# Kernel optimization log

Hardware: AMD Instinct MI355X
Metric: run time of the kernel (lower is better)

## Reference

```python
import jax, jax.numpy as jnp
import numpy as np

N_ENTITIES = 80000
N_EDGES = 1280000
N_RELATIONS = 50
EMB = 64


def setup_inputs() -> dict:
    key = jax.random.key(0)
    k1, k2, k3, k4 = jax.random.split(key, 4)
    entity_emb = jax.random.normal(k1, (N_ENTITIES, EMB), dtype=jnp.float32)
    edge_index = jax.random.randint(k2, (2, N_EDGES), 0, N_ENTITIES, dtype=jnp.int64)
    edge_type = jax.random.randint(k3, (N_EDGES,), 0, N_RELATIONS, dtype=jnp.int64)
    relation_emb = jax.random.normal(k4, (N_RELATIONS, EMB), dtype=jnp.float32)
    return {
        "entity_emb": entity_emb,
        "edge_index": edge_index,
        "edge_type": edge_type,
        "relation_emb": relation_emb,
        "n_entities": N_ENTITIES,
    }


def reference(entity_emb, edge_index, edge_type, relation_emb, n_entities):
    head, tail = edge_index[0], edge_index[1]          # [E], [E]
    rel = relation_emb[edge_type]                      # [E, D] gather
    head_emb = entity_emb[head]                        # [E, D] gather
    tail_emb = entity_emb[tail]                        # [E, D] gather
    # per-edge dot-product score over head * relation * tail
    scores = jnp.sum(head_emb * rel * tail_emb, axis=-1)  # [E]
    # segment softmax over edges grouped by head (numerically stable)
    seg_max = jax.ops.segment_max(scores, head, num_segments=n_entities)  # [N]
    ex = jnp.exp(scores - seg_max[head])                                  # [E]
    seg_sum = jax.ops.segment_sum(ex, head, num_segments=n_entities)     # [N]
    attn = ex / seg_sum[head]                                             # [E]
    # weighted scatter-sum of tail embeddings into head slots
    entity_agg = jax.ops.segment_sum(tail_emb * attn[:, None], head,
                                     num_segments=n_entities)             # [N, D]
    return entity_agg
```

## Files before the change

### kernel.cpp

```cpp
#include <hip/hip_runtime.h>
#include <hip/hip_fp16.h>


#define NBK        1250
#define BCAP       1280
#define EDGE_TILE4 4096

__device__ __forceinline__ int f2i(float x) { return __builtin_bit_cast(int, x); }
__device__ __forceinline__ float i2f(int x) { return __builtin_bit_cast(float, x); }

template <int N>
__device__ __forceinline__ float dpp_ror_add(float x) {
    int y = __builtin_amdgcn_update_dpp(0, f2i(x), 0x120 + N, 0xF, 0xF, true);
    return x + i2f(y);
}
__device__ __forceinline__ float swz16(float x) {
    return i2f(__builtin_amdgcn_ds_swizzle(f2i(x), 0x401F));
}
__device__ __forceinline__ float bperm(int ba, float x) {
    return i2f(__builtin_amdgcn_ds_bpermute(ba, f2i(x)));
}

__device__ __forceinline__ uint2 pk4h(float4 v) {
    unsigned a = __builtin_bit_cast(unsigned short, __float2half_rn(v.x));
    unsigned b = __builtin_bit_cast(unsigned short, __float2half_rn(v.y));
    unsigned c = __builtin_bit_cast(unsigned short, __float2half_rn(v.z));
    unsigned d = __builtin_bit_cast(unsigned short, __float2half_rn(v.w));
    uint2 o; o.x = a | (b << 16); o.y = c | (d << 16); return o;
}

__global__ void cvt_kernel(const float* __restrict__ ent,
                           unsigned* __restrict__ enth, int NF4) {
    const float4* src = (const float4*)ent;
    uint2* dst = (uint2*)enth;
    for (int i = blockIdx.x * blockDim.x + threadIdx.x; i < NF4;
         i += gridDim.x * blockDim.x)
        dst[i] = pk4h(src[i]);
}

__global__ void __launch_bounds__(1024)
pass1_kernel(const int* __restrict__ edge, const int* __restrict__ etype,
             int* __restrict__ bcur, int* __restrict__ mid, int E, int E4) {
    __shared__ int lh[1280];
    __shared__ int lbase[1280];
    int tid = threadIdx.x;
    lh[tid] = 0;
    if (tid < NBK - 1024) lh[1024 + tid] = 0;
    __syncthreads();

    const int4* H = (const int4*)edge;
    const int4* T = (const int4*)(edge + E);
    const int4* R = (const int4*)etype;
    int base = blockIdx.x * EDGE_TILE4;

    int4 ent4[4];
    int4 rb4[4];
    bool valid[4];
    #pragma unroll
    for (int r = 0; r < 4; ++r) {
        int idx4 = base + r * 1024 + tid;
        valid[r] = (idx4 < E4);
        if (valid[r]) {
            int4 h = H[idx4];
            int4 t = T[idx4];
            int4 rl = R[idx4];
            int b, rk;
            b = h.x >> 6; rk = atomicAdd(&lh[b], 1);
            ent4[r].x = ((h.x & 63) << 23) | (rl.x << 17) | t.x;
            rb4[r].x = b | (rk << 11);
            b = h.y >> 6; rk = atomicAdd(&lh[b], 1);
            ent4[r].y = ((h.y & 63) << 23) | (rl.y << 17) | t.y;
            rb4[r].y = b | (rk << 11);
            b = h.z >> 6; rk = atomicAdd(&lh[b], 1);
            ent4[r].z = ((h.z & 63) << 23) | (rl.z << 17) | t.z;
            rb4[r].z = b | (rk << 11);
            b = h.w >> 6; rk = atomicAdd(&lh[b], 1);
            ent4[r].w = ((h.w & 63) << 23) | (rl.w << 17) | t.w;
            rb4[r].w = b | (rk << 11);
        }
    }
    __syncthreads();
    {
        int i = tid;
        lbase[i] = lh[i] ? atomicAdd(&bcur[i], lh[i]) : 0;
        if (tid < NBK - 1024) {
            i = 1024 + tid;
            lbase[i] = lh[i] ? atomicAdd(&bcur[i], lh[i]) : 0;
        }
    }
    __syncthreads();
    #pragma unroll
    for (int r = 0; r < 4; ++r) {
        if (valid[r]) {
            int b, pos;
            b = rb4[r].x & 2047; pos = lbase[b] + ((unsigned)rb4[r].x >> 11);
            mid[b * BCAP + min(pos, BCAP - 1)] = ent4[r].x;
            b = rb4[r].y & 2047; pos = lbase[b] + ((unsigned)rb4[r].y >> 11);
            mid[b * BCAP + min(pos, BCAP - 1)] = ent4[r].y;
            b = rb4[r].z & 2047; pos = lbase[b] + ((unsigned)rb4[r].z >> 11);
            mid[b * BCAP + min(pos, BCAP - 1)] = ent4[r].z;
            b = rb4[r].w & 2047; pos = lbase[b] + ((unsigned)rb4[r].w >> 11);
            mid[b * BCAP + min(pos, BCAP - 1)] = ent4[r].w;
        }
    }
}

__global__ void __launch_bounds__(512)
bucket_agg_kernel(const float* __restrict__ ent,
                  const unsigned* __restrict__ enth,
                  const float* __restrict__ rel,
                  const int* __restrict__ bcur,
                  const int* __restrict__ mid,
                  float* __restrict__ out) {
    __shared__ int    sh_sorted[BCAP + 32];
    __shared__ float4 srel[850];
    __shared__ int    sh_hist[64];
    __shared__ int    sh_cur[64];
    __shared__ int    sh_start[65];
    __shared__ int    sh_hpop;

    int b   = blockIdx.x;
    int tid = threadIdx.x;
    int beg = b * BCAP;
    int n   = bcur[b];
    if (n > BCAP) n = BCAP;

    for (int r = tid; r < 800; r += 512)
        srel[(r >> 4) * 17 + (r & 15)] = ((const float4*)rel)[r];
    if (tid < 64) sh_hist[tid] = 0;
    if (tid == 0) sh_hpop = 0;
    __syncthreads();

    for (int i = tid; i < n; i += 512)
        atomicAdd(&sh_hist[(unsigned)mid[beg + i] >> 23], 1);
    __syncthreads();
    if (tid < 64) sh_cur[tid] = sh_hist[tid];
    __syncthreads();
    #pragma unroll
    for (int d = 1; d < 64; d <<= 1) {
        int u = 0;
        if (tid < 64 && tid >= d) u = sh_cur[tid - d];
        __syncthreads();
        if (tid < 64) sh_cur[tid] += u;
        __syncthreads();
    }
    if (tid < 64) {
        int ex = sh_cur[tid] - sh_hist[tid];
        sh_start[tid] = ex;
        sh_cur[tid] = ex;
        if (tid == 63) sh_start[64] = n;
    }
    if (tid < 32) sh_sorted[n + tid] = 0;
    __syncthreads();
    for (int i = tid; i < n; i += 512) {
        int e = mid[beg + i];
        int pos = atomicAdd(&sh_cur[(unsigned)e >> 23], 1);
        sh_sorted[pos] = (((e >> 17) & 63) << 24) | ((e & 0x1FFFF) << 7);
    }
    __syncthreads();

    int lane = tid & 63;
    int g = lane >> 4;
    int l = lane & 15;
    const char* entl = (const char*)enth + (l << 3);
    const float LOG2E = 1.44269504088896340736f;
    int head_base = b << 6;
    int pad_end = n + 16;

    for (;;) {
        int hl = 0;
        if (lane == 0) hl = atomicAdd(&sh_hpop, 1);
        hl = __shfl(hl, 0);
        if (hl >= 64) break;
        int s = sh_start[hl];
        int c = sh_start[hl + 1] - s;
        int head = head_base + hl;
        float4 hr = ((const float4*)ent)[(size_t)head * 16 + l];
        float hx = hr.x * LOG2E, hy = hr.y * LOG2E;
        float hz = hr.z * LOG2E, hw = hr.w * LOG2E;
        float ssum = 0.0f;
        float4 acc = make_float4(0.f, 0.f, 0.f, 0.f);

        int T = (c + 15) >> 4;
        int   pvA[4]; uint2 twA[4];
        int   pvB[4]; uint2 twB[4];
        #pragma unroll
        for (int j = 0; j < 4; ++j) {
            int idx = s + g + 4 * j;
            idx = (idx < pad_end) ? idx : pad_end - 1;
            pvA[j] = sh_sorted[idx];
            twA[j] = *(const uint2*)(entl + (pvA[j] & 0x00FFFF80));
        }
        for (int it = 0; it < T; ++it) {
            if (it + 1 < T) {
                #pragma unroll
                for (int j = 0; j < 4; ++j) {
                    int idx = s + g + 4 * (4 * (it + 1) + j);
                    idx = (idx < pad_end) ? idx : pad_end - 1;
                    pvB[j] = sh_sorted[idx];
                    twB[j] = *(const uint2*)(entl + (pvB[j] & 0x00FFFF80));
                }
            }
            #pragma unroll
            for (int j = 0; j < 4; ++j) {
                float2 f0 = __half22float2(__builtin_bit_cast(__half2, twA[j].x));
                float2 f1 = __half22float2(__builtin_bit_cast(__half2, twA[j].y));
                float4 rv = srel[((unsigned)pvA[j] >> 24) * 17 + l];
                float p = hx * rv.x * f0.x;
                p = fmaf(hy * rv.y, f0.y, p);
                p = fmaf(hz * rv.z, f1.x, p);
                p = fmaf(hw * rv.w, f1.y, p);
                p = dpp_ror_add<1>(p);
                p = dpp_ror_add<2>(p);
                p = dpp_ror_add<4>(p);
                p = dpp_ror_add<8>(p);
                p = (g + 4 * (4 * it + j) < c) ? p : -3.0e38f;
                float e2 = __builtin_amdgcn_exp2f(p);
                ssum += e2;
                acc.x = fmaf(e2, f0.x, acc.x);
                acc.y = fmaf(e2, f0.y, acc.y);
                acc.z = fmaf(e2, f1.x, acc.z);
                acc.w = fmaf(e2, f1.y, acc.w);
            }
            #pragma unroll
            for (int j = 0; j < 4; ++j) { pvA[j] = pvB[j]; twA[j] = twB[j]; }
        }
        ssum  += swz16(ssum);
        acc.x += swz16(acc.x);
        acc.y += swz16(acc.y);
        acc.z += swz16(acc.z);
        acc.w += swz16(acc.w);
        int ba = (lane ^ 32) << 2;
        ssum  += bperm(ba, ssum);
        acc.x += bperm(ba, acc.x);
        acc.y += bperm(ba, acc.y);
        acc.z += bperm(ba, acc.z);
        acc.w += bperm(ba, acc.w);

        if (g == 0) {
            float inv = (c > 0) ? 1.0f / ssum : 0.0f;
            ((float4*)out)[(size_t)head * 16 + l] =
                make_float4(acc.x * inv, acc.y * inv, acc.z * inv, acc.w * inv);
        }
    }
}

extern "C" void kernel_launch(void* const* d_in, const int* in_sizes, int n_in,
                              void* d_out, int out_size, void* d_ws, size_t ws_size,
                              hipStream_t stream) {
    const float* ent   = (const float*)d_in[0];
    const int*   edge  = (const int*)d_in[1];
    const int*   etype = (const int*)d_in[2];
    const float* rel   = (const float*)d_in[3];
    int E = in_sizes[1] / 2;
    int N = out_size / 64;
    float* out = (float*)d_out;

    int* bcur      = (int*)d_ws;
    unsigned* enth = (unsigned*)(bcur + NBK);
    int* mid       = (int*)(enth + (size_t)N * 32);

    hipMemsetAsync(bcur, 0, (size_t)NBK * sizeof(int), stream);

    int E4 = E / 4;
    int NF4 = N * 16;
    int nblk = (E4 + EDGE_TILE4 - 1) / EDGE_TILE4;
    cvt_kernel<<<512, 256, 0, stream>>>(ent, enth, NF4);
    pass1_kernel<<<nblk, 1024, 0, stream>>>(edge, etype, bcur, mid, E, E4);
    bucket_agg_kernel<<<NBK, 512, 0, stream>>>(ent, enth, rel, bcur, mid, out);
}
```

Measured before the change: 82.72 us.

## Fuse fp16 conversion into pass1 and make bucket aggregation persistent

The entity fp32-to-fp16 conversion is folded into the pass1 binning kernel, which removes one kernel launch. The bucket aggregation kernel becomes persistent: a fixed grid of 1024 blocks pulls buckets from a global atomic counter, so the relation table is staged into shared memory once per block instead of once per bucket. The tail index clamp on the shared sorted list is dropped because the padding already covers over-reads. A side effect is that inserting the counter shifts the fp16 entity buffer by 4 bytes, so its 8-byte vector loads may be misaligned, and pass1's small grid now has to do the conversion work as well.

```diff
diff --git a/kernel.cpp b/kernel.cpp
--- a/kernel.cpp
+++ b/kernel.cpp
@@ -5,6 +5,7 @@
 #define NBK        1250
 #define BCAP       1280
 #define EDGE_TILE4 4096
+#define AGG_BLOCKS 1024
 
 __device__ __forceinline__ int f2i(float x) { return __builtin_bit_cast(int, x); }
 __device__ __forceinline__ float i2f(int x) { return __builtin_bit_cast(float, x); }
@@ -29,23 +30,23 @@
     uint2 o; o.x = a | (b << 16); o.y = c | (d << 16); return o;
 }
 
-__global__ void cvt_kernel(const float* __restrict__ ent,
-                           unsigned* __restrict__ enth, int NF4) {
-    const float4* src = (const float4*)ent;
-    uint2* dst = (uint2*)enth;
-    for (int i = blockIdx.x * blockDim.x + threadIdx.x; i < NF4;
-         i += gridDim.x * blockDim.x)
-        dst[i] = pk4h(src[i]);
-}
-
 __global__ void __launch_bounds__(1024)
 pass1_kernel(const int* __restrict__ edge, const int* __restrict__ etype,
-             int* __restrict__ bcur, int* __restrict__ mid, int E, int E4) {
+             const float* __restrict__ ent, unsigned* __restrict__ enth,
+             int* __restrict__ bcur, int* __restrict__ mid,
+             int E, int E4, int NF4) {
     __shared__ int lh[1280];
     __shared__ int lbase[1280];
     int tid = threadIdx.x;
     lh[tid] = 0;
     if (tid < NBK - 1024) lh[1024 + tid] = 0;
+
+    {
+        const float4* src = (const float4*)ent;
+        uint2* dst = (uint2*)enth;
+        for (int i = blockIdx.x * 1024 + tid; i < NF4; i += gridDim.x * 1024)
+            dst[i] = pk4h(src[i]);
+    }
     __syncthreads();
 
     const int4* H = (const int4*)edge;
@@ -111,6 +112,7 @@
                   const float* __restrict__ rel,
                   const int* __restrict__ bcur,
                   const int* __restrict__ mid,
+                  int* __restrict__ wk,
                   float* __restrict__ out) {
     __shared__ int    sh_sorted[BCAP + 32];
     __shared__ float4 srel[850];
@@ -118,130 +120,132 @@
     __shared__ int    sh_cur[64];
     __shared__ int    sh_start[65];
     __shared__ int    sh_hpop;
-
-    int b   = blockIdx.x;
+    __shared__ int    sh_bkt;
+
     int tid = threadIdx.x;
-    int beg = b * BCAP;
-    int n   = bcur[b];
-    if (n > BCAP) n = BCAP;
-
     for (int r = tid; r < 800; r += 512)
         srel[(r >> 4) * 17 + (r & 15)] = ((const float4*)rel)[r];
-    if (tid < 64) sh_hist[tid] = 0;
-    if (tid == 0) sh_hpop = 0;
-    __syncthreads();
-
-    for (int i = tid; i < n; i += 512)
-        atomicAdd(&sh_hist[(unsigned)mid[beg + i] >> 23], 1);
-    __syncthreads();
-    if (tid < 64) sh_cur[tid] = sh_hist[tid];
-    __syncthreads();
-    #pragma unroll
-    for (int d = 1; d < 64; d <<= 1) {
-        int u = 0;
-        if (tid < 64 && tid >= d) u = sh_cur[tid - d];
-        __syncthreads();
-        if (tid < 64) sh_cur[tid] += u;
-        __syncthreads();
-    }
-    if (tid < 64) {
-        int ex = sh_cur[tid] - sh_hist[tid];
-        sh_start[tid] = ex;
-        sh_cur[tid] = ex;
-        if (tid == 63) sh_start[64] = n;
-    }
-    if (tid < 32) sh_sorted[n + tid] = 0;
-    __syncthreads();
-    for (int i = tid; i < n; i += 512) {
-        int e = mid[beg + i];
-        int pos = atomicAdd(&sh_cur[(unsigned)e >> 23], 1);
-        sh_sorted[pos] = (((e >> 17) & 63) << 24) | ((e & 0x1FFFF) << 7);
-    }
-    __syncthreads();
 
     int lane = tid & 63;
     int g = lane >> 4;
     int l = lane & 15;
     const char* entl = (const char*)enth + (l << 3);
     const float LOG2E = 1.44269504088896340736f;
-    int head_base = b << 6;
-    int pad_end = n + 16;
 
     for (;;) {
-        int hl = 0;
-        if (lane == 0) hl = atomicAdd(&sh_hpop, 1);
-        hl = __shfl(hl, 0);
-        if (hl >= 64) break;
-        int s = sh_start[hl];
-        int c = sh_start[hl + 1] - s;
-        int head = head_base + hl;
-        float4 hr = ((const float4*)ent)[(size_t)head * 16 + l];
-        float hx = hr.x * LOG2E, hy = hr.y * LOG2E;
-        float hz = hr.z * LOG2E, hw = hr.w * LOG2E;
-        float ssum = 0.0f;
-        float4 acc = make_float4(0.f, 0.f, 0.f, 0.f);
-
-        int T = (c + 15) >> 4;
-        int   pvA[4]; uint2 twA[4];
-        int   pvB[4]; uint2 twB[4];
+        if (tid == 0) sh_bkt = atomicAdd(wk, 1);
+        if (tid < 64) sh_hist[tid] = 0;
+        if (tid == 65) sh_hpop = 0;
+        __syncthreads();
+        int b = sh_bkt;
+        if (b >= NBK) break;
+        int beg = b * BCAP;
+        int n   = bcur[b];
+        if (n > BCAP) n = BCAP;
+
+        for (int i = tid; i < n; i += 512)
+            atomicAdd(&sh_hist[(unsigned)mid[beg + i] >> 23], 1);
+        __syncthreads();
+        if (tid < 64) sh_cur[tid] = sh_hist[tid];
+        __syncthreads();
         #pragma unroll
-        for (int j = 0; j < 4; ++j) {
-            int idx = s + g + 4 * j;
-            idx = (idx < pad_end) ? idx : pad_end - 1;
-            pvA[j] = sh_sorted[idx];
-            twA[j] = *(const uint2*)(entl + (pvA[j] & 0x00FFFF80));
-        }
-        for (int it = 0; it < T; ++it) {
-            if (it + 1 < T) {
+        for (int d = 1; d < 64; d <<= 1) {
+            int u = 0;
+            if (tid < 64 && tid >= d) u = sh_cur[tid - d];
+            __syncthreads();
+            if (tid < 64) sh_cur[tid] += u;
+            __syncthreads();
+        }
+        if (tid < 64) {
+            int ex = sh_cur[tid] - sh_hist[tid];
+            sh_start[tid] = ex;
+            sh_cur[tid] = ex;
+            if (tid == 63) sh_start[64] = n;
+        }
+        if (tid < 32) sh_sorted[n + tid] = 0;
+        __syncthreads();
+        for (int i = tid; i < n; i += 512) {
+            int e = mid[beg + i];
+            int pos = atomicAdd(&sh_cur[(unsigned)e >> 23], 1);
+            sh_sorted[pos] = (((e >> 17) & 63) << 24) | ((e & 0x1FFFF) << 7);
+        }
+        __syncthreads();
+
+        int head_base = b << 6;
+        for (;;) {
+            int hl = 0;
+            if (lane == 0) hl = atomicAdd(&sh_hpop, 1);
+            hl = __shfl(hl, 0);
+            if (hl >= 64) break;
+            int s = sh_start[hl];
+            int c = sh_start[hl + 1] - s;
+            int head = head_base + hl;
+            float4 hr = ((const float4*)ent)[(size_t)head * 16 + l];
+            float hx = hr.x * LOG2E, hy = hr.y * LOG2E;
+            float hz = hr.z * LOG2E, hw = hr.w * LOG2E;
+            float ssum = 0.0f;
+            float4 acc = make_float4(0.f, 0.f, 0.f, 0.f);
+
+            int T = (c + 15) >> 4;
+            int   pvA[4]; uint2 twA[4];
+            int   pvB[4]; uint2 twB[4];
+            #pragma unroll
+            for (int j = 0; j < 4; ++j) {
+                pvA[j] = sh_sorted[s + g + 4 * j];
+                twA[j] = *(const uint2*)(entl + (pvA[j] & 0x00FFFF80));
+            }
+            for (int it = 0; it < T; ++it) {
+                if (it + 1 < T) {
+                    #pragma unroll
+                    for (int j = 0; j < 4; ++j) {
+                        pvB[j] = sh_sorted[s + g + 4 * (4 * (it + 1) + j)];
+                        twB[j] = *(const uint2*)(entl + (pvB[j] & 0x00FFFF80));
+                    }
+                }
                 #pragma unroll
                 for (int j = 0; j < 4; ++j) {
-                    int idx = s + g + 4 * (4 * (it + 1) + j);
-                    idx = (idx < pad_end) ? idx : pad_end - 1;
-                    pvB[j] = sh_sorted[idx];
-                    twB[j] = *(const uint2*)(entl + (pvB[j] & 0x00FFFF80));
+                    float2 f0 = __half22float2(__builtin_bit_cast(__half2, twA[j].x));
+                    float2 f1 = __half22float2(__builtin_bit_cast(__half2, twA[j].y));
+                    float4 rv = srel[((unsigned)pvA[j] >> 24) * 17 + l];
+                    float p = hx * rv.x * f0.x;
+                    p = fmaf(hy * rv.y, f0.y, p);
+                    p = fmaf(hz * rv.z, f1.x, p);
+                    p = fmaf(hw * rv.w, f1.y, p);
+                    p = dpp_ror_add<1>(p);
+                    p = dpp_ror_add<2>(p);
+                    p = dpp_ror_add<4>(p);
+                    p = dpp_ror_add<8>(p);
+                    p = (g + 4 * (4 * it + j) < c) ? p : -3.0e38f;
+                    float e2 = __builtin_amdgcn_exp2f(p);
+                    ssum += e2;
+                    acc.x = fmaf(e2, f0.x, acc.x);
+                    acc.y = fmaf(e2, f0.y, acc.y);
+                    acc.z = fmaf(e2, f1.x, acc.z);
+                    acc.w = fmaf(e2, f1.y, acc.w);
                 }
+                #pragma unroll
+                for (int j = 0; j < 4; ++j) { pvA[j] = pvB[j]; twA[j] = twB[j]; }
             }
-            #pragma unroll
-            for (int j = 0; j < 4; ++j) {
-                float2 f0 = __half22float2(__builtin_bit_cast(__half2, twA[j].x));
-                float2 f1 = __half22float2(__builtin_bit_cast(__half2, twA[j].y));
-                float4 rv = srel[((unsigned)pvA[j] >> 24) * 17 + l];
-                float p = hx * rv.x * f0.x;
-                p = fmaf(hy * rv.y, f0.y, p);
-                p = fmaf(hz * rv.z, f1.x, p);
-                p = fmaf(hw * rv.w, f1.y, p);
-                p = dpp_ror_add<1>(p);
-                p = dpp_ror_add<2>(p);
-                p = dpp_ror_add<4>(p);
-                p = dpp_ror_add<8>(p);
-                p = (g + 4 * (4 * it + j) < c) ? p : -3.0e38f;
-                float e2 = __builtin_amdgcn_exp2f(p);
-                ssum += e2;
-                acc.x = fmaf(e2, f0.x, acc.x);
-                acc.y = fmaf(e2, f0.y, acc.y);
-                acc.z = fmaf(e2, f1.x, acc.z);
-                acc.w = fmaf(e2, f1.y, acc.w);
+            ssum  += swz16(ssum);
+            acc.x += swz16(acc.x);
+            acc.y += swz16(acc.y);
+            acc.z += swz16(acc.z);
+            acc.w += swz16(acc.w);
+            int ba = (lane ^ 32) << 2;
+            ssum  += bperm(ba, ssum);
+            acc.x += bperm(ba, acc.x);
+            acc.y += bperm(ba, acc.y);
+            acc.z += bperm(ba, acc.z);
+            acc.w += bperm(ba, acc.w);
+
+            if (g == 0) {
+                float inv = (c > 0) ? 1.0f / ssum : 0.0f;
+                ((float4*)out)[(size_t)head * 16 + l] =
+                    make_float4(acc.x * inv, acc.y * inv,
+                                acc.z * inv, acc.w * inv);
             }
-            #pragma unroll
-            for (int j = 0; j < 4; ++j) { pvA[j] = pvB[j]; twA[j] = twB[j]; }
-        }
-        ssum  += swz16(ssum);
-        acc.x += swz16(acc.x);
-        acc.y += swz16(acc.y);
-        acc.z += swz16(acc.z);
-        acc.w += swz16(acc.w);
-        int ba = (lane ^ 32) << 2;
-        ssum  += bperm(ba, ssum);
-        acc.x += bperm(ba, acc.x);
-        acc.y += bperm(ba, acc.y);
-        acc.z += bperm(ba, acc.z);
-        acc.w += bperm(ba, acc.w);
-
-        if (g == 0) {
-            float inv = (c > 0) ? 1.0f / ssum : 0.0f;
-            ((float4*)out)[(size_t)head * 16 + l] =
-                make_float4(acc.x * inv, acc.y * inv, acc.z * inv, acc.w * inv);
-        }
+        }
+        __syncthreads();
     }
 }
 
@@ -257,15 +261,17 @@
     float* out = (float*)d_out;
 
     int* bcur      = (int*)d_ws;
-    unsigned* enth = (unsigned*)(bcur + NBK);
+    int* wk        = bcur + NBK;
+    unsigned* enth = (unsigned*)(wk + 1);
     int* mid       = (int*)(enth + (size_t)N * 32);
 
-    hipMemsetAsync(bcur, 0, (size_t)NBK * sizeof(int), stream);
+    hipMemsetAsync(bcur, 0, (size_t)(NBK + 1) * sizeof(int), stream);
 
     int E4 = E / 4;
     int NF4 = N * 16;
     int nblk = (E4 + EDGE_TILE4 - 1) / EDGE_TILE4;
-    cvt_kernel<<<512, 256, 0, stream>>>(ent, enth, NF4);
-    pass1_kernel<<<nblk, 1024, 0, stream>>>(edge, etype, bcur, mid, E, E4);
-    bucket_agg_kernel<<<NBK, 512, 0, stream>>>(ent, enth, rel, bcur, mid, out);
-}
+    pass1_kernel<<<nblk, 1024, 0, stream>>>(edge, etype, ent, enth, bcur, mid,
+                                            E, E4, NF4);
+    bucket_agg_kernel<<<AGG_BLOCKS, 512, 0, stream>>>(ent, enth, rel, bcur,
+                                                      mid, wk, out);
+}
```

After: 142.9 us. 1.73x slower.
